# Kernel optimization log

Hardware: AMD Instinct MI355X
Metric: run time of the kernel (lower is better)

## Reference

```python
import jax, jax.numpy as jnp
import numpy as np

N = 30000      # nodes
E = 480000     # edges (before self loops)
DIN = 128      # dim_in
DH = 32        # dim_h (per-head out channels)
H1 = 8         # gat1 heads
H2 = 2         # gat2 heads
G = 64         # num graphs in batch
DOUT = 10      # dim_out
NEG_SLOPE = 0.2


def _glorot(key, shape):
    fan_in = shape[0]
    return jax.random.normal(key, shape, dtype=jnp.float32) / np.sqrt(fan_in)


def setup_inputs() -> dict:
    key = jax.random.key(0)
    ks = jax.random.split(key, 16)
    x = jax.random.normal(ks[0], (N, DIN), dtype=jnp.float32)
    edge_index = jax.random.randint(ks[1], (2, E), 0, N, dtype=jnp.int32)
    batch = jnp.sort(jax.random.randint(ks[2], (N,), 0, G, dtype=jnp.int32))
    # GATv2Conv layer 1: lin_l, lin_r (dim_in -> H1*DH), att (H1, DH), bias (H1*DH)
    W1l = _glorot(ks[3], (DIN, H1 * DH))
    W1r = _glorot(ks[4], (DIN, H1 * DH))
    a1 = _glorot(ks[5], (DH, H1)).T  # [H1, DH]
    b1 = jnp.zeros((H1 * DH,), dtype=jnp.float32)
    # GATv2Conv layer 2: (H1*DH -> H2*DH)
    W2l = _glorot(ks[6], (H1 * DH, H2 * DH))
    W2r = _glorot(ks[7], (H1 * DH, H2 * DH))
    a2 = _glorot(ks[8], (DH, H2)).T  # [H2, DH]
    b2 = jnp.zeros((H2 * DH,), dtype=jnp.float32)
    # MLP head: fc1(2*DH -> DH), fc2(DH -> DH//2), fc(DH//2 -> DOUT); stored [in,out]
    fc1_w = _glorot(ks[9], (2 * DH, DH)); fc1_b = jnp.zeros((DH,), jnp.float32)
    fc2_w = _glorot(ks[10], (DH, DH // 2)); fc2_b = jnp.zeros((DH // 2,), jnp.float32)
    fc_w = _glorot(ks[11], (DH // 2, DOUT)); fc_b = jnp.zeros((DOUT,), jnp.float32)
    return {"x": x, "edge_index": edge_index, "batch": batch,
            "W1l": W1l, "W1r": W1r, "a1": a1, "b1": b1,
            "W2l": W2l, "W2r": W2r, "a2": a2, "b2": b2,
            "fc1_w": fc1_w, "fc1_b": fc1_b, "fc2_w": fc2_w, "fc2_b": fc2_b,
            "fc_w": fc_w, "fc_b": fc_b}


def gatv2_conv(x, edge_index, Wl, Wr, att, bias, heads, dh, n):
    """PyG GATv2Conv: concat=True, add_self_loops=True, negative_slope=0.2."""
    src, dst = edge_index[0], edge_index[1]
    loop = jnp.arange(n, dtype=src.dtype)        # self loops (PyG default)
    src = jnp.concatenate([src, loop])
    dst = jnp.concatenate([dst, loop])
    xl = (x @ Wl).reshape(n, heads, dh)          # source transform
    xr = (x @ Wr).reshape(n, heads, dh)          # destination transform
    xj = xl[src]                                  # [Etot, H, dh] message features
    s = jax.nn.leaky_relu(xj + xr[dst], NEG_SLOPE)
    e = jnp.einsum('ehd,hd->eh', s, att)          # per-edge per-head score
    # segment softmax over incoming edges of each destination node
    m = jax.ops.segment_max(e, dst, num_segments=n)
    p = jnp.exp(e - m[dst])
    z = jax.ops.segment_sum(p, dst, num_segments=n)
    alpha = p / z[dst]                            # [Etot, H]
    out = jax.ops.segment_sum(xj * alpha[..., None], dst, num_segments=n)
    return out.reshape(n, heads * dh) + bias


def reference(x, edge_index, batch, W1l, W1r, a1, b1, W2l, W2r, a2, b2,
              fc1_w, fc1_b, fc2_w, fc2_b, fc_w, fc_b):
    h = gatv2_conv(x, edge_index, W1l, W1r, a1, b1, H1, DH, N)
    h = jax.nn.elu(h)
    h = gatv2_conv(h, edge_index, W2l, W2r, a2, b2, H2, DH, N)  # [N, 2*DH]
    # global_mean_pool
    sums = jax.ops.segment_sum(h, batch, num_segments=G)
    cnt = jax.ops.segment_sum(jnp.ones((N,), h.dtype), batch, num_segments=G)
    hg = sums / jnp.maximum(cnt, 1.0)[:, None]    # [G, 2*DH]
    x1 = jax.nn.relu(hg @ fc1_w + fc1_b)
    # dropout p=0.2 is identity in eval mode
    x2 = jax.nn.relu(x1 @ fc2_w + fc2_b)
    c = x2 @ fc_w + fc_b
    return (c, x2)
```

## Files before the change

kernel.cpp:

```cpp
#include <hip/hip_runtime.h>
#include <math.h>

#define DIN 128
#define DH  32
#define H1  8
#define H2  2
#define GNUM 64
#define DOUT 10
#define NEG_SLOPE 0.2f
#define SCAN_B 512

typedef __attribute__((ext_vector_type(8))) short sv8;
typedef __attribute__((ext_vector_type(4))) float fv4;

static __device__ __forceinline__ unsigned short f2bf(float f) {
    unsigned int u = __float_as_uint(f);
    unsigned int r = (u + 0x7fffu + ((u >> 16) & 1u)) >> 16;
    return (unsigned short)r;
}
static __device__ __forceinline__ float bf2f(unsigned short h) {
    return __uint_as_float(((unsigned int)h) << 16);
}


__global__ void k_prep(const float* __restrict__ x,
                       const float* __restrict__ W1l, const float* __restrict__ W1r,
                       const float* __restrict__ W2l, const float* __restrict__ W2r,
                       unsigned short* __restrict__ xgh, unsigned short* __restrict__ xgl,
                       short* __restrict__ B1th, short* __restrict__ B1tl,
                       short* __restrict__ B2th, short* __restrict__ B2tl,
                       int* __restrict__ zbase, int nz, int n) {
    int id = blockIdx.x * blockDim.x + threadIdx.x;
    if (id < nz) zbase[id] = 0;
    const int NX = n * 32;
    const int T1 = 512 * 128;
    const int T2 = 128 * 256;
    if (id < NX) {
        int m = id >> 5, j4 = id & 31;
        float4 v = *(const float4*)(x + (size_t)m * 128 + j4 * 4);
        unsigned short hx = f2bf(v.x), hy = f2bf(v.y), hz = f2bf(v.z), hw = f2bf(v.w);
        ushort4 hi; hi.x = hx; hi.y = hy; hi.z = hz; hi.w = hw;
        ushort4 lo;
        lo.x = f2bf(v.x - bf2f(hx)); lo.y = f2bf(v.y - bf2f(hy));
        lo.z = f2bf(v.z - bf2f(hz)); lo.w = f2bf(v.w - bf2f(hw));
        int R = m >> 4, r = m & 15;
        int C = j4 >> 3, q = (j4 >> 1) & 3, j = (j4 & 1) * 4;
        size_t o = ((size_t)(R * 4 + C) * 64 + q * 16 + r) * 8 + j;
        *(ushort4*)(xgh + o) = hi;
        *(ushort4*)(xgl + o) = lo;
    } else if (id < NX + T1) {
        int id1 = id - NX;
        int nn = id1 / 128, k = id1 - nn * 128;
        float v = (nn < 256) ? W1l[(size_t)k * 256 + nn] : W1r[(size_t)k * 256 + (nn - 256)];
        unsigned short h = f2bf(v);
        size_t o = (((size_t)(nn >> 4) * 4 + (k >> 5)) * 64 + ((k >> 3) & 3) * 16 + (nn & 15)) * 8 + (k & 7);
        B1th[o] = (short)h;
        B1tl[o] = (short)f2bf(v - bf2f(h));
    } else if (id < NX + T1 + T2) {
        int id2 = id - NX - T1;
        int nn = id2 / 256, k = id2 - nn * 256;
        float v = (nn < 64) ? W2l[(size_t)k * 64 + nn] : W2r[(size_t)k * 64 + (nn - 64)];
        unsigned short h = f2bf(v);
        size_t o = (((size_t)(nn >> 4) * 8 + (k >> 5)) * 64 + ((k >> 3) & 3) * 16 + (nn & 15)) * 8 + (k & 7);
        B2th[o] = (short)h;
        B2tl[o] = (short)f2bf(v - bf2f(h));
    }
}

__global__ void k_deg(const int* __restrict__ dst, int* __restrict__ deg, int E, int n) {
    int i = blockIdx.x * blockDim.x + threadIdx.x;
    if (i < E) {
        atomicAdd(&deg[dst[i]], 1);
    } else if (i < E + n) {
        atomicAdd(&deg[i - E], 1);
    }
}

__global__ __launch_bounds__(SCAN_B)
void k_scan_partial(const int* __restrict__ deg, int* __restrict__ bsum, int n) {
    int i = blockIdx.x * SCAN_B + threadIdx.x;
    int v = (i < n) ? deg[i] : 0;
    #pragma unroll
    for (int m = 32; m >= 1; m >>= 1) v += __shfl_xor(v, m);
    __shared__ int red[SCAN_B / 64];
    if ((threadIdx.x & 63) == 0) red[threadIdx.x >> 6] = v;
    __syncthreads();
    if (threadIdx.x == 0) {
        int s = 0;
        #pragma unroll
        for (int k = 0; k < SCAN_B / 64; ++k) s += red[k];
        bsum[blockIdx.x] = s;
    }
}

__global__ __launch_bounds__(SCAN_B)
void k_scan_apply(int* __restrict__ deg, int* __restrict__ cursor,
                  const int* __restrict__ bsum, int n, int nb) {
    __shared__ int buf[SCAN_B];
    __shared__ int pfx_s, tot_s;
    const int t = threadIdx.x, b = blockIdx.x;
    if (t < 64) {
        int v = (t < nb) ? bsum[t] : 0;
        int incl = v;
        #pragma unroll
        for (int o = 1; o < 64; o <<= 1) {
            int w = __shfl_up(incl, o);
            if (t >= o) incl += w;
        }
        int pfx = (b == 0) ? 0 : __shfl(incl, b - 1);
        int tot = __shfl(incl, nb - 1);
        if (t == 0) { pfx_s = pfx; tot_s = tot; }
    }
    int i = b * SCAN_B + t;
    int v = (i < n) ? deg[i] : 0;
    buf[t] = v;
    __syncthreads();
    for (int o = 1; o < SCAN_B; o <<= 1) {
        int a = (t >= o) ? buf[t - o] : 0;
        __syncthreads();
        buf[t] += a;
        __syncthreads();
    }
    int excl = buf[t] - v + pfx_s;
    if (i < n) { deg[i] = excl; cursor[i] = excl; }
    if (b == 0 && t == 0) deg[n] = tot_s;
}

__global__ void k_scatter(const int* __restrict__ src, const int* __restrict__ dst,
                          int* __restrict__ cursor, int* __restrict__ csr_src, int E, int n) {
    int i = blockIdx.x * blockDim.x + threadIdx.x;
    if (i < E) {
        int d = dst[i];
        int pos = atomicAdd(&cursor[d], 1);
        csr_src[pos] = src[i];
    } else if (i < E + n) {
        int v = i - E;
        int pos = atomicAdd(&cursor[v], 1);
        csr_src[pos] = v;
    }
}

__global__ __launch_bounds__(256, 2)
void k_gemm1(const unsigned short* __restrict__ Ah, const unsigned short* __restrict__ Al,
             const short* __restrict__ Bth, const short* __restrict__ Btl,
             unsigned short* __restrict__ C,
             int M, int Ntot) {
    __shared__ float smc[64 * 68];
    const int tid = threadIdx.x;
    const int lane = tid & 63;
    const int wid = tid >> 6;
    const int wm = wid & 1, wn = wid >> 1;
    const int m0 = blockIdx.x * 128;
    const int n0 = blockIdx.y * 128;
    const int l15 = lane & 15, q = lane >> 4;
    const int MR = (M >> 4) - 1;

    fv4 acc[4][4] = {};

    const unsigned short* ap[4];
    const unsigned short* alp[4];
    #pragma unroll
    for (int fm = 0; fm < 4; ++fm) {
        int R = (m0 >> 4) + wm * 4 + fm;
        if (R > MR) R = MR;
        ap[fm]  = Ah + ((size_t)R * 4 * 64 + lane) * 8;
        alp[fm] = Al + ((size_t)R * 4 * 64 + lane) * 8;
    }
    const short* bhp[4];
    const short* blp[4];
    #pragma unroll
    for (int fn = 0; fn < 4; ++fn) {
        int R = (n0 >> 4) + wn * 4 + fn;
        bhp[fn] = Bth + ((size_t)R * 4 * 64 + lane) * 8;
        blp[fn] = Btl + ((size_t)R * 4 * 64 + lane) * 8;
    }

    #pragma unroll
    for (int c = 0; c < 4; ++c) {
        const size_t co = (size_t)c * 512;
        sv8 ah[4], al[4], bh[4], bl[4];
        #pragma unroll
        for (int fn = 0; fn < 4; ++fn) {
            bh[fn] = *(const sv8*)(bhp[fn] + co);
            bl[fn] = *(const sv8*)(blp[fn] + co);
        }
        #pragma unroll
        for (int fm = 0; fm < 4; ++fm) {
            ah[fm] = *(const sv8*)(ap[fm] + co);
            al[fm] = *(const sv8*)(alp[fm] + co);
        }
        #pragma unroll
        for (int fm = 0; fm < 4; ++fm) {
            #pragma unroll
            for (int fn = 0; fn < 4; ++fn) {
                acc[fm][fn] = __builtin_amdgcn_mfma_f32_16x16x32_bf16(ah[fm], bh[fn], acc[fm][fn], 0, 0, 0);
                acc[fm][fn] = __builtin_amdgcn_mfma_f32_16x16x32_bf16(ah[fm], bl[fn], acc[fm][fn], 0, 0, 0);
                acc[fm][fn] = __builtin_amdgcn_mfma_f32_16x16x32_bf16(al[fm], bh[fn], acc[fm][fn], 0, 0, 0);
            }
        }
    }

    #pragma unroll
    for (int s = 0; s < 2; ++s) {
        #pragma unroll
        for (int cn = 0; cn < 2; ++cn) {
            __syncthreads();
            if (wm == s && wn == cn) {
                #pragma unroll
                for (int fm = 0; fm < 4; ++fm)
                    #pragma unroll
                    for (int fn = 0; fn < 4; ++fn)
                        #pragma unroll
                        for (int r = 0; r < 4; ++r)
                            smc[(fm * 16 + q * 4 + r) * 68 + fn * 16 + l15] = acc[fm][fn][r];
            }
            __syncthreads();
            int lr = tid >> 2;
            int grow = m0 + s * 64 + lr;
            if (grow < M) {
                #pragma unroll
                for (int k4 = 0; k4 < 4; ++k4) {
                    int jj = (tid & 3) + k4 * 4;
                    float4 vv = *(float4*)&smc[lr * 68 + jj * 4];
                    int gcol = n0 + cn * 64 + jj * 4;
                    ushort4 uu;
                    uu.x = f2bf(vv.x); uu.y = f2bf(vv.y);
                    uu.z = f2bf(vv.z); uu.w = f2bf(vv.w);
                    *(ushort4*)(C + (size_t)grow * Ntot + gcol) = uu;
                }
            }
        }
    }
}

__global__ __launch_bounds__(256, 2)
void k_gemm_bf(const unsigned short* __restrict__ A, const short* __restrict__ Bth,
               const short* __restrict__ Btl,
               unsigned short* __restrict__ C,
               int M, int Ntot) {
    __shared__ float smc[64 * 36];
    const int tid = threadIdx.x;
    const int lane = tid & 63;
    const int wid = tid >> 6;
    const int wm = wid & 1, wn = wid >> 1;
    const int m0 = blockIdx.x * 128;
    const int n0 = blockIdx.y * 64;
    const int l15 = lane & 15, q = lane >> 4;
    const int MR = (M >> 4) - 1;

    fv4 acc[4][2] = {};

    const unsigned short* ap[4];
    #pragma unroll
    for (int fm = 0; fm < 4; ++fm) {
        int R = (m0 >> 4) + wm * 4 + fm;
        if (R > MR) R = MR;
        ap[fm] = A + ((size_t)R * 8 * 64 + lane) * 8;
    }
    const short* bhp[2];
    const short* blp[2];
    #pragma unroll
    for (int fn = 0; fn < 2; ++fn) {
        int R = (n0 >> 4) + wn * 2 + fn;
        bhp[fn] = Bth + ((size_t)R * 8 * 64 + lane) * 8;
        blp[fn] = Btl + ((size_t)R * 8 * 64 + lane) * 8;
    }

    #pragma unroll 4
    for (int c = 0; c < 8; ++c) {
        const size_t co = (size_t)c * 512;
        sv8 ah[4], bh[2], bl[2];
        #pragma unroll
        for (int fn = 0; fn < 2; ++fn) {
            bh[fn] = *(const sv8*)(bhp[fn] + co);
            bl[fn] = *(const sv8*)(blp[fn] + co);
        }
        #pragma unroll
        for (int fm = 0; fm < 4; ++fm)
            ah[fm] = *(const sv8*)(ap[fm] + co);
        #pragma unroll
        for (int fm = 0; fm < 4; ++fm) {
            #pragma unroll
            for (int fn = 0; fn < 2; ++fn) {
                acc[fm][fn] = __builtin_amdgcn_mfma_f32_16x16x32_bf16(ah[fm], bh[fn], acc[fm][fn], 0, 0, 0);
                acc[fm][fn] = __builtin_amdgcn_mfma_f32_16x16x32_bf16(ah[fm], bl[fn], acc[fm][fn], 0, 0, 0);
            }
        }
    }

    #pragma unroll
    for (int s = 0; s < 2; ++s) {
        #pragma unroll
        for (int cn = 0; cn < 2; ++cn) {
            __syncthreads();
            if (wm == s && wn == cn) {
                #pragma unroll
                for (int fm = 0; fm < 4; ++fm)
                    #pragma unroll
                    for (int fn = 0; fn < 2; ++fn)
                        #pragma unroll
                        for (int r = 0; r < 4; ++r)
                            smc[(fm * 16 + q * 4 + r) * 36 + fn * 16 + l15] = acc[fm][fn][r];
            }
            __syncthreads();
            int lr = tid >> 2;
            int grow = m0 + s * 64 + lr;
            if (grow < M) {
                #pragma unroll
                for (int k4 = 0; k4 < 2; ++k4) {
                    int jj = (tid & 3) + k4 * 4;
                    float4 vv = *(float4*)&smc[lr * 36 + jj * 4];
                    int gcol = n0 + cn * 32 + jj * 4;
                    ushort4 uu;
                    uu.x = f2bf(vv.x); uu.y = f2bf(vv.y);
                    uu.z = f2bf(vv.z); uu.w = f2bf(vv.w);
                    *(ushort4*)(C + (size_t)grow * Ntot + gcol) = uu;
                }
            }
        }
    }
}

__global__ __launch_bounds__(256)
void k_edge1(const unsigned short* __restrict__ XLR,
             const int* __restrict__ offs, const int* __restrict__ csr,
             const float* __restrict__ att, const float* __restrict__ bias,
             unsigned short* __restrict__ out, int n) {
    const int tid = threadIdx.x;
    const int lane = tid & 63;
    const int v = blockIdx.x * 4 + (tid >> 6);
    if (v >= n) return;
    const int li = lane & 31;
    const int half = lane >> 5;
    const uint4* XL4 = (const uint4*)XLR;
    float av[8], xr[8];
    #pragma unroll
    for (int k = 0; k < 8; ++k) av[k] = att[li * 8 + k];
    {
        uint4 u = XL4[(size_t)v * 64 + 32 + li];
        xr[0] = __uint_as_float(u.x << 16);  xr[1] = __uint_as_float(u.x & 0xffff0000u);
        xr[2] = __uint_as_float(u.y << 16);  xr[3] = __uint_as_float(u.y & 0xffff0000u);
        xr[4] = __uint_as_float(u.z << 16);  xr[5] = __uint_as_float(u.z & 0xffff0000u);
        xr[6] = __uint_as_float(u.w << 16);  xr[7] = __uint_as_float(u.w & 0xffff0000u);
    }
    float z = 0.f;
    float acc[8] = {};
    const int e0 = offs[v], e1 = offs[v + 1];

    int j = e0 + half;
    bool val = (j < e1);
    int jj = val ? j : (e1 - 1);
    int src = csr[jj];
    uint4 u = XL4[(size_t)src * 64 + li];

    for (int base = e0; base < e1; base += 2) {
        int jn = j + 2;
        bool valn = (jn < e1);
        int jjn = valn ? jn : (e1 - 1);
        int srcn = csr[jjn];
        uint4 un = XL4[(size_t)srcn * 64 + li];

        float f[8];
        f[0] = __uint_as_float(u.x << 16);  f[1] = __uint_as_float(u.x & 0xffff0000u);
        f[2] = __uint_as_float(u.y << 16);  f[3] = __uint_as_float(u.y & 0xffff0000u);
        f[4] = __uint_as_float(u.z << 16);  f[5] = __uint_as_float(u.z & 0xffff0000u);
        f[6] = __uint_as_float(u.w << 16);  f[7] = __uint_as_float(u.w & 0xffff0000u);
        float s1 = 0.f, s2 = 0.f;
        #pragma unroll
        for (int k = 0; k < 8; ++k) {
            float t = f[k] + xr[k];
            s1 = fmaf(t, av[k], s1);
            s2 = fmaf(fabsf(t), av[k], s2);
        }
        float s = fmaf(0.6f, s1, 0.4f * s2);
        s += __shfl_xor(s, 1);
        s += __shfl_xor(s, 2);
        float w = val ? __expf(s) : 0.f;
        z += w;
        #pragma unroll
        for (int k = 0; k < 8; ++k) acc[k] = fmaf(w, f[k], acc[k]);

        u = un; val = valn; j = jn;
    }
    z += __shfl_xor(z, 32);
    #pragma unroll
    for (int k = 0; k < 8; ++k) acc[k] += __shfl_xor(acc[k], 32);
    if (half == 0) {
        const float rz = 1.f / z;
        unsigned int o[4];
        #pragma unroll
        for (int k2 = 0; k2 < 4; ++k2) {
            float lo = fmaf(acc[k2 * 2 + 0], rz, bias[li * 8 + k2 * 2 + 0]);
            float hi = fmaf(acc[k2 * 2 + 1], rz, bias[li * 8 + k2 * 2 + 1]);
            lo = (lo > 0.f) ? lo : (__expf(lo) - 1.f);
            hi = (hi > 0.f) ? hi : (__expf(hi) - 1.f);
            o[k2] = (unsigned int)f2bf(lo) | ((unsigned int)f2bf(hi) << 16);
        }
        uint4 ov = { o[0], o[1], o[2], o[3] };
        size_t po = (((size_t)(v >> 4) * 8 + (li >> 2)) * 64 + (li & 3) * 16 + (v & 15)) * 8;
        *(uint4*)(out + po) = ov;
    }
}

__global__ __launch_bounds__(256)
void k_edge2(const unsigned short* __restrict__ XLR,
             const int* __restrict__ offs, const int* __restrict__ csr,
             const float* __restrict__ att, const float* __restrict__ bias,
             float* __restrict__ out, int n) {
    const int tid = threadIdx.x;
    const int lane = tid & 63;
    const int v = blockIdx.x * 4 + (tid >> 6);
    if (v >= n) return;
    const int li = lane & 7;
    const int slot = lane >> 3;
    const uint4* XL4 = (const uint4*)XLR;
    float av[8], xr[8];
    #pragma unroll
    for (int k = 0; k < 8; ++k) av[k] = att[li * 8 + k];
    {
        uint4 u = XL4[(size_t)v * 16 + 8 + li];
        xr[0] = __uint_as_float(u.x << 16);  xr[1] = __uint_as_float(u.x & 0xffff0000u);
        xr[2] = __uint_as_float(u.y << 16);  xr[3] = __uint_as_float(u.y & 0xffff0000u);
        xr[4] = __uint_as_float(u.z << 16);  xr[5] = __uint_as_float(u.z & 0xffff0000u);
        xr[6] = __uint_as_float(u.w << 16);  xr[7] = __uint_as_float(u.w & 0xffff0000u);
    }
    float z = 0.f;
    float acc[8] = {};
    const int e0 = offs[v], e1 = offs[v + 1];

    int j = e0 + slot;
    bool val = (j < e1);
    int jj = val ? j : (e1 - 1);
    int src = csr[jj];
    uint4 u = XL4[(size_t)src * 16 + li];

    for (int base = e0; base < e1; base += 8) {
        int jn = j + 8;
        bool valn = (jn < e1);
        int jjn = valn ? jn : (e1 - 1);
        int srcn = csr[jjn];
        uint4 un = XL4[(size_t)srcn * 16 + li];

        float f[8];
        f[0] = __uint_as_float(u.x << 16);  f[1] = __uint_as_float(u.x & 0xffff0000u);
        f[2] = __uint_as_float(u.y << 16);  f[3] = __uint_as_float(u.y & 0xffff0000u);
        f[4] = __uint_as_float(u.z << 16);  f[5] = __uint_as_float(u.z & 0xffff0000u);
        f[6] = __uint_as_float(u.w << 16);  f[7] = __uint_as_float(u.w & 0xffff0000u);
        float s1 = 0.f, s2 = 0.f;
        #pragma unroll
        for (int k = 0; k < 8; ++k) {
            float t = f[k] + xr[k];
            s1 = fmaf(t, av[k], s1);
            s2 = fmaf(fabsf(t), av[k], s2);
        }
        float s = fmaf(0.6f, s1, 0.4f * s2);
        s += __shfl_xor(s, 1);
        s += __shfl_xor(s, 2);
        float w = val ? __expf(s) : 0.f;
        z += w;
        #pragma unroll
        for (int k = 0; k < 8; ++k) acc[k] = fmaf(w, f[k], acc[k]);

        u = un; val = valn; j = jn;
    }
    z += __shfl_xor(z, 8);  z += __shfl_xor(z, 16);  z += __shfl_xor(z, 32);
    #pragma unroll
    for (int k = 0; k < 8; ++k) {
        acc[k] += __shfl_xor(acc[k], 8);
        acc[k] += __shfl_xor(acc[k], 16);
        acc[k] += __shfl_xor(acc[k], 32);
    }
    if (slot == 0) {
        const float rz = 1.f / z;
        float o[8];
        #pragma unroll
        for (int k = 0; k < 8; ++k)
            o[k] = fmaf(acc[k], rz, bias[li * 8 + k]);
        float4 o0 = { o[0], o[1], o[2], o[3] };
        float4 o1 = { o[4], o[5], o[6], o[7] };
        *(float4*)(out + (size_t)v * 64 + li * 8 + 0) = o0;
        *(float4*)(out + (size_t)v * 64 + li * 8 + 4) = o1;
    }
}

__global__ __launch_bounds__(256)
void k_pool_mlp(const float* __restrict__ out2, const int* __restrict__ batch,
                const float* __restrict__ fc1w, const float* __restrict__ fc1b,
                const float* __restrict__ fc2w, const float* __restrict__ fc2b,
                const float* __restrict__ fcw,  const float* __restrict__ fcb,
                float* __restrict__ outc, float* __restrict__ outx2, int n) {
    const int g = blockIdx.x;
    const int t = threadIdx.x;
    const int lane = t & 63;
    const int w = t >> 6;
    __shared__ float red[4][64];
    __shared__ float hg_s[64];
    __shared__ float x1_s[32];
    __shared__ float x2_s[16];

    int lo = 0, hi = n;
    while (lo < hi) { int mid = (lo + hi) >> 1; if (batch[mid] < g) lo = mid + 1; else hi = mid; }
    const int start = lo;
    hi = n;
    while (lo < hi) { int mid = (lo + hi) >> 1; if (batch[mid] < g + 1) lo = mid + 1; else hi = mid; }
    const int end = lo;

    float s = 0.f;
    for (int v = start + w; v < end; v += 4)
        s += out2[(size_t)v * 64 + lane];
    red[w][lane] = s;
    __syncthreads();
    if (w == 0) {
        float tot = red[0][lane] + red[1][lane] + red[2][lane] + red[3][lane];
        float cnt = fmaxf((float)(end - start), 1.0f);
        hg_s[lane] = tot / cnt;
    }
    __syncthreads();
    if (t < 32) {
        float a = fc1b[t];
        #pragma unroll
        for (int k = 0; k < 64; ++k) a = fmaf(hg_s[k], fc1w[k * 32 + t], a);
        x1_s[t] = fmaxf(a, 0.f);
    }
    __syncthreads();
    if (t < 16) {
        float a = fc2b[t];
        #pragma unroll
        for (int k = 0; k < 32; ++k) a = fmaf(x1_s[k], fc2w[k * 16 + t], a);
        x2_s[t] = fmaxf(a, 0.f);
    }
    __syncthreads();
    if (t < DOUT) {
        float a = fcb[t];
        #pragma unroll
        for (int k = 0; k < 16; ++k) a = fmaf(x2_s[k], fcw[k * 10 + t], a);
        outc[g * DOUT + t] = a;
    }
    if (t < 16) outx2[g * 16 + t] = x2_s[t];
}

extern "C" void kernel_launch(void* const* d_in, const int* in_sizes, int n_in,
                              void* d_out, int out_size, void* d_ws, size_t ws_size,
                              hipStream_t stream) {
    const float* x    = (const float*)d_in[0];
    const int*   ei   = (const int*)d_in[1];
    const int*   batch= (const int*)d_in[2];
    const float* W1l  = (const float*)d_in[3];
    const float* W1r  = (const float*)d_in[4];
    const float* a1   = (const float*)d_in[5];
    const float* b1   = (const float*)d_in[6];
    const float* W2l  = (const float*)d_in[7];
    const float* W2r  = (const float*)d_in[8];
    const float* a2   = (const float*)d_in[9];
    const float* b2   = (const float*)d_in[10];
    const float* fc1w = (const float*)d_in[11];
    const float* fc1b = (const float*)d_in[12];
    const float* fc2w = (const float*)d_in[13];
    const float* fc2b = (const float*)d_in[14];
    const float* fcw  = (const float*)d_in[15];
    const float* fcb  = (const float*)d_in[16];

    const int N = in_sizes[2];
    const int E = in_sizes[1] / 2;
    const int ET = E + N;
    const int* esrc = ei;
    const int* edst = ei + E;
    const int NB = (N + SCAN_B - 1) / SCAN_B;

    char* ws = (char*)d_ws;
    size_t off = 0;
    unsigned short* xlr1b = (unsigned short*)(ws + off); off += (size_t)N * 512 * 2;
    unsigned short* h1b  = (unsigned short*)(ws + off);  off += (size_t)N * 256 * 2;
    float* out2 = (float*)(ws + off);            off += (size_t)N * 64 * 4;
    int*   deg   = (int*)(ws + off);             off += ((size_t)(N + 1) * 4 + 255) & ~255ull;
    int*   cursor= (int*)(ws + off);             off += ((size_t)N * 4 + 255) & ~255ull;
    int*   csr   = (int*)(ws + off);             off += ((size_t)ET * 4 + 255) & ~255ull;
    int*   bsum  = (int*)(ws + off);             off += ((size_t)(NB + 1) * 4 + 255) & ~255ull;
    short* B1th  = (short*)(ws + off);           off += (size_t)512 * 128 * 2;
    short* B1tl  = (short*)(ws + off);           off += (size_t)512 * 128 * 2;
    short* B2th  = (short*)(ws + off);           off += (size_t)128 * 256 * 2;
    short* B2tl  = (short*)(ws + off);           off += (size_t)128 * 256 * 2;
    unsigned short* xgh = (unsigned short*)(ws + off); off += (size_t)N * 128 * 2;
    unsigned short* xgl = (unsigned short*)(ws + off); off += (size_t)N * 128 * 2;
    unsigned short* xlr2b = xlr1b;
    (void)ws_size; (void)n_in; (void)out_size;

    float* outc  = (float*)d_out;
    float* outx2 = (float*)d_out + GNUM * DOUT;

    const int prep_tot = N * 32 + 512 * 128 + 128 * 256;
    k_prep<<<(prep_tot + 255) / 256, 256, 0, stream>>>(
        x, W1l, W1r, W2l, W2r, xgh, xgl, B1th, B1tl, B2th, B2tl, deg, N + 1, N);

    int tb = 256;
    int gb = (ET + tb - 1) / tb;
    k_deg<<<gb, tb, 0, stream>>>(edst, deg, E, N);
    k_scan_partial<<<NB, SCAN_B, 0, stream>>>(deg, bsum, N);
    k_scan_apply<<<NB, SCAN_B, 0, stream>>>(deg, cursor, bsum, N, NB);
    k_scatter<<<gb, tb, 0, stream>>>(esrc, edst, cursor, csr, E, N);

    dim3 g1((N + 127) / 128, 4);
    k_gemm1<<<g1, 256, 0, stream>>>(xgh, xgl, B1th, B1tl, xlr1b, N, 512);

    k_edge1<<<(N + 3) / 4, 256, 0, stream>>>(xlr1b, deg, csr, a1, b1, h1b, N);

    dim3 g2((N + 127) / 128, 2);
    k_gemm_bf<<<g2, 256, 0, stream>>>(h1b, B2th, B2tl, xlr2b, N, 128);

    k_edge2<<<(N + 3) / 4, 256, 0, stream>>>(xlr2b, deg, csr, a2, b2, out2, N);

    k_pool_mlp<<<GNUM, 256, 0, stream>>>(out2, batch, fc1w, fc1b, fc2w, fc2b,
                                         fcw, fcb, outc, outx2, N);
}
```

Measured before the change: 275.2 us.

## Split XL/XR buffers, deepen gather prefetch, and pack edge math into float2 ops

The combined XL|XR projection buffer is split into separate contiguous XL and XR arrays, so edge gathers read a compact 256- or 64-wide row instead of striding over 512- or 128-wide rows. The GEMM epilogues now stage a full 128-row tile in shared memory with fewer barriers and store 16-byte packed bf16 using v_cvt_pk_bf16_f32. The edge kernels prefetch two iterations ahead and use packed float2 FMA/max/min arithmetic for leaky-ReLU scoring. The log2e factor is folded into the attention weights so exp2 can replace exp. Shared memory per GEMM block doubles, which may affect occupancy.

```diff
diff --git a/kernel.cpp b/kernel.cpp
--- a/kernel.cpp
+++ b/kernel.cpp
@@ -12,6 +12,7 @@
 
 typedef __attribute__((ext_vector_type(8))) short sv8;
 typedef __attribute__((ext_vector_type(4))) float fv4;
+typedef __attribute__((ext_vector_type(2))) float f32x2;
 
 static __device__ __forceinline__ unsigned short f2bf(float f) {
     unsigned int u = __float_as_uint(f);
@@ -20,6 +21,17 @@
 }
 static __device__ __forceinline__ float bf2f(unsigned short h) {
     return __uint_as_float(((unsigned int)h) << 16);
+}
+static __device__ __forceinline__ unsigned int cvtpk(float lo, float hi) {
+    unsigned int r;
+    asm("v_cvt_pk_bf16_f32 %0, %1, %2" : "=v"(r) : "v"(lo), "v"(hi));
+    return r;
+}
+static __device__ __forceinline__ f32x2 up2(unsigned int w) {
+    f32x2 r;
+    r.x = __uint_as_float(w << 16);
+    r.y = __uint_as_float(w & 0xffff0000u);
+    return r;
 }
 
 
@@ -143,9 +155,9 @@
 __global__ __launch_bounds__(256, 2)
 void k_gemm1(const unsigned short* __restrict__ Ah, const unsigned short* __restrict__ Al,
              const short* __restrict__ Bth, const short* __restrict__ Btl,
-             unsigned short* __restrict__ C,
-             int M, int Ntot) {
-    __shared__ float smc[64 * 68];
+             unsigned short* __restrict__ XLo, unsigned short* __restrict__ XRo,
+             int M) {
+    __shared__ float smc[128 * 68];
     const int tid = threadIdx.x;
     const int lane = tid & 63;
     const int wid = tid >> 6;
@@ -201,33 +213,33 @@
     }
 
     #pragma unroll
-    for (int s = 0; s < 2; ++s) {
-        #pragma unroll
-        for (int cn = 0; cn < 2; ++cn) {
-            __syncthreads();
-            if (wm == s && wn == cn) {
+    for (int p = 0; p < 2; ++p) {
+        if (p) __syncthreads();
+        if (wn == p) {
+            #pragma unroll
+            for (int fm = 0; fm < 4; ++fm)
                 #pragma unroll
-                for (int fm = 0; fm < 4; ++fm)
+                for (int fn = 0; fn < 4; ++fn)
                     #pragma unroll
-                    for (int fn = 0; fn < 4; ++fn)
-                        #pragma unroll
-                        for (int r = 0; r < 4; ++r)
-                            smc[(fm * 16 + q * 4 + r) * 68 + fn * 16 + l15] = acc[fm][fn][r];
-            }
-            __syncthreads();
-            int lr = tid >> 2;
-            int grow = m0 + s * 64 + lr;
-            if (grow < M) {
-                #pragma unroll
-                for (int k4 = 0; k4 < 4; ++k4) {
-                    int jj = (tid & 3) + k4 * 4;
-                    float4 vv = *(float4*)&smc[lr * 68 + jj * 4];
-                    int gcol = n0 + cn * 64 + jj * 4;
-                    ushort4 uu;
-                    uu.x = f2bf(vv.x); uu.y = f2bf(vv.y);
-                    uu.z = f2bf(vv.z); uu.w = f2bf(vv.w);
-                    *(ushort4*)(C + (size_t)grow * Ntot + gcol) = uu;
-                }
+                    for (int r = 0; r < 4; ++r)
+                        smc[(wm * 64 + fm * 16 + q * 4 + r) * 68 + fn * 16 + l15] = acc[fm][fn][r];
+        }
+        __syncthreads();
+        int lr = tid >> 1;
+        int ch = (tid & 1) * 32;
+        int grow = m0 + lr;
+        if (grow < M) {
+            int colb = n0 + p * 64 + ch;
+            unsigned short* dst = (colb < 256)
+                ? XLo + (size_t)grow * 256 + colb
+                : XRo + (size_t)grow * 256 + (colb - 256);
+            #pragma unroll
+            for (int j = 0; j < 4; ++j) {
+                float4 a = *(float4*)&smc[lr * 68 + ch + j * 8];
+                float4 b = *(float4*)&smc[lr * 68 + ch + j * 8 + 4];
+                uint4 o = { cvtpk(a.x, a.y), cvtpk(a.z, a.w),
+                            cvtpk(b.x, b.y), cvtpk(b.z, b.w) };
+                *(uint4*)(dst + j * 8) = o;
             }
         }
     }
@@ -236,9 +248,9 @@
 __global__ __launch_bounds__(256, 2)
 void k_gemm_bf(const unsigned short* __restrict__ A, const short* __restrict__ Bth,
                const short* __restrict__ Btl,
-               unsigned short* __restrict__ C,
-               int M, int Ntot) {
-    __shared__ float smc[64 * 36];
+               unsigned short* __restrict__ XL2, unsigned short* __restrict__ XR2,
+               int M) {
+    __shared__ float smc[128 * 36];
     const int tid = threadIdx.x;
     const int lane = tid & 63;
     const int wid = tid >> 6;
@@ -289,40 +301,40 @@
     }
 
     #pragma unroll
-    for (int s = 0; s < 2; ++s) {
-        #pragma unroll
-        for (int cn = 0; cn < 2; ++cn) {
-            __syncthreads();
-            if (wm == s && wn == cn) {
+    for (int p = 0; p < 2; ++p) {
+        if (p) __syncthreads();
+        if (wn == p) {
+            #pragma unroll
+            for (int fm = 0; fm < 4; ++fm)
                 #pragma unroll
-                for (int fm = 0; fm < 4; ++fm)
+                for (int fn = 0; fn < 2; ++fn)
                     #pragma unroll
-                    for (int fn = 0; fn < 2; ++fn)
-                        #pragma unroll
-                        for (int r = 0; r < 4; ++r)
-                            smc[(fm * 16 + q * 4 + r) * 36 + fn * 16 + l15] = acc[fm][fn][r];
+                    for (int r = 0; r < 4; ++r)
+                        smc[(wm * 64 + fm * 16 + q * 4 + r) * 36 + fn * 16 + l15] = acc[fm][fn][r];
+        }
+        __syncthreads();
+        int lr = tid >> 1;
+        int ch = (tid & 1) * 16;
+        int grow = m0 + lr;
+        if (grow < M) {
+            int colb = n0 + p * 32 + ch;
+            unsigned short* dst = (colb < 64)
+                ? XL2 + (size_t)grow * 64 + colb
+                : XR2 + (size_t)grow * 64 + (colb - 64);
+            #pragma unroll
+            for (int j = 0; j < 2; ++j) {
+                float4 a = *(float4*)&smc[lr * 36 + ch + j * 8];
+                float4 b = *(float4*)&smc[lr * 36 + ch + j * 8 + 4];
+                uint4 o = { cvtpk(a.x, a.y), cvtpk(a.z, a.w),
+                            cvtpk(b.x, b.y), cvtpk(b.z, b.w) };
+                *(uint4*)(dst + j * 8) = o;
             }
-            __syncthreads();
-            int lr = tid >> 2;
-            int grow = m0 + s * 64 + lr;
-            if (grow < M) {
-                #pragma unroll
-                for (int k4 = 0; k4 < 2; ++k4) {
-                    int jj = (tid & 3) + k4 * 4;
-                    float4 vv = *(float4*)&smc[lr * 36 + jj * 4];
-                    int gcol = n0 + cn * 32 + jj * 4;
-                    ushort4 uu;
-                    uu.x = f2bf(vv.x); uu.y = f2bf(vv.y);
-                    uu.z = f2bf(vv.z); uu.w = f2bf(vv.w);
-                    *(ushort4*)(C + (size_t)grow * Ntot + gcol) = uu;
-                }
-            }
         }
     }
 }
 
 __global__ __launch_bounds__(256)
-void k_edge1(const unsigned short* __restrict__ XLR,
+void k_edge1(const unsigned short* __restrict__ XL, const unsigned short* __restrict__ XR,
              const int* __restrict__ offs, const int* __restrict__ csr,
              const float* __restrict__ att, const float* __restrict__ bias,
              unsigned short* __restrict__ out, int n) {
@@ -332,69 +344,83 @@
     if (v >= n) return;
     const int li = lane & 31;
     const int half = lane >> 5;
-    const uint4* XL4 = (const uint4*)XLR;
-    float av[8], xr[8];
-    #pragma unroll
-    for (int k = 0; k < 8; ++k) av[k] = att[li * 8 + k];
+    const uint4* XL4 = (const uint4*)XL;
+    const uint4* XR4 = (const uint4*)XR;
+    const float LOG2E = 1.4426950408889634f;
+    f32x2 av[4], xr[4];
+    #pragma unroll
+    for (int k = 0; k < 4; ++k) {
+        av[k].x = att[li * 8 + 2 * k] * LOG2E;
+        av[k].y = att[li * 8 + 2 * k + 1] * LOG2E;
+    }
     {
-        uint4 u = XL4[(size_t)v * 64 + 32 + li];
-        xr[0] = __uint_as_float(u.x << 16);  xr[1] = __uint_as_float(u.x & 0xffff0000u);
-        xr[2] = __uint_as_float(u.y << 16);  xr[3] = __uint_as_float(u.y & 0xffff0000u);
-        xr[4] = __uint_as_float(u.z << 16);  xr[5] = __uint_as_float(u.z & 0xffff0000u);
-        xr[6] = __uint_as_float(u.w << 16);  xr[7] = __uint_as_float(u.w & 0xffff0000u);
+        uint4 u = XR4[(size_t)v * 32 + li];
+        xr[0] = up2(u.x); xr[1] = up2(u.y); xr[2] = up2(u.z); xr[3] = up2(u.w);
     }
     float z = 0.f;
-    float acc[8] = {};
+    f32x2 acc[4] = {};
     const int e0 = offs[v], e1 = offs[v + 1];
-
-    int j = e0 + half;
-    bool val = (j < e1);
-    int jj = val ? j : (e1 - 1);
-    int src = csr[jj];
-    uint4 u = XL4[(size_t)src * 64 + li];
-
+    const int el = e1 - 1;
+
+    int j0 = e0 + half;
+    int c0 = csr[j0 < e1 ? j0 : el];
+    uint4 u0 = XL4[(size_t)c0 * 32 + li];
+    int j1 = j0 + 2;
+    int c1 = csr[j1 < e1 ? j1 : el];
+    uint4 u1 = XL4[(size_t)c1 * 32 + li];
+    int j2 = j0 + 4;
+    int c2 = csr[j2 < e1 ? j2 : el];
+
+    #pragma unroll 2
     for (int base = e0; base < e1; base += 2) {
-        int jn = j + 2;
-        bool valn = (jn < e1);
-        int jjn = valn ? jn : (e1 - 1);
-        int srcn = csr[jjn];
-        uint4 un = XL4[(size_t)srcn * 64 + li];
-
-        float f[8];
-        f[0] = __uint_as_float(u.x << 16);  f[1] = __uint_as_float(u.x & 0xffff0000u);
-        f[2] = __uint_as_float(u.y << 16);  f[3] = __uint_as_float(u.y & 0xffff0000u);
-        f[4] = __uint_as_float(u.z << 16);  f[5] = __uint_as_float(u.z & 0xffff0000u);
-        f[6] = __uint_as_float(u.w << 16);  f[7] = __uint_as_float(u.w & 0xffff0000u);
-        float s1 = 0.f, s2 = 0.f;
-        #pragma unroll
-        for (int k = 0; k < 8; ++k) {
-            float t = f[k] + xr[k];
-            s1 = fmaf(t, av[k], s1);
-            s2 = fmaf(fabsf(t), av[k], s2);
-        }
-        float s = fmaf(0.6f, s1, 0.4f * s2);
+        uint4 u2 = XL4[(size_t)c2 * 32 + li];
+        int j3 = j2 + 2;
+        int c3 = csr[j3 < e1 ? j3 : el];
+
+        f32x2 f0 = up2(u0.x), f1 = up2(u0.y), f2 = up2(u0.z), f3 = up2(u0.w);
+        const f32x2 zz = { 0.f, 0.f };
+        f32x2 sp = zz, sm = zz, t;
+        t = f0 + xr[0];
+        sp = __builtin_elementwise_fma(__builtin_elementwise_max(t, zz), av[0], sp);
+        sm = __builtin_elementwise_fma(__builtin_elementwise_min(t, zz), av[0], sm);
+        t = f1 + xr[1];
+        sp = __builtin_elementwise_fma(__builtin_elementwise_max(t, zz), av[1], sp);
+        sm = __builtin_elementwise_fma(__builtin_elementwise_min(t, zz), av[1], sm);
+        t = f2 + xr[2];
+        sp = __builtin_elementwise_fma(__builtin_elementwise_max(t, zz), av[2], sp);
+        sm = __builtin_elementwise_fma(__builtin_elementwise_min(t, zz), av[2], sm);
+        t = f3 + xr[3];
+        sp = __builtin_elementwise_fma(__builtin_elementwise_max(t, zz), av[3], sp);
+        sm = __builtin_elementwise_fma(__builtin_elementwise_min(t, zz), av[3], sm);
+        float s = (sp.x + sp.y) + 0.2f * (sm.x + sm.y);
         s += __shfl_xor(s, 1);
         s += __shfl_xor(s, 2);
-        float w = val ? __expf(s) : 0.f;
+        float w = (j0 < e1) ? exp2f(s) : 0.f;
         z += w;
-        #pragma unroll
-        for (int k = 0; k < 8; ++k) acc[k] = fmaf(w, f[k], acc[k]);
-
-        u = un; val = valn; j = jn;
+        f32x2 ww = { w, w };
+        acc[0] = __builtin_elementwise_fma(f0, ww, acc[0]);
+        acc[1] = __builtin_elementwise_fma(f1, ww, acc[1]);
+        acc[2] = __builtin_elementwise_fma(f2, ww, acc[2]);
+        acc[3] = __builtin_elementwise_fma(f3, ww, acc[3]);
+
+        u0 = u1; u1 = u2;
+        j0 = j1; j1 = j2; j2 = j3; c2 = c3;
     }
     z += __shfl_xor(z, 32);
-    #pragma unroll
-    for (int k = 0; k < 8; ++k) acc[k] += __shfl_xor(acc[k], 32);
+    float a8[8] = { acc[0].x, acc[0].y, acc[1].x, acc[1].y,
+                    acc[2].x, acc[2].y, acc[3].x, acc[3].y };
+    #pragma unroll
+    for (int k = 0; k < 8; ++k) a8[k] += __shfl_xor(a8[k], 32);
     if (half == 0) {
         const float rz = 1.f / z;
         unsigned int o[4];
         #pragma unroll
         for (int k2 = 0; k2 < 4; ++k2) {
-            float lo = fmaf(acc[k2 * 2 + 0], rz, bias[li * 8 + k2 * 2 + 0]);
-            float hi = fmaf(acc[k2 * 2 + 1], rz, bias[li * 8 + k2 * 2 + 1]);
+            float lo = fmaf(a8[2 * k2 + 0], rz, bias[li * 8 + 2 * k2 + 0]);
+            float hi = fmaf(a8[2 * k2 + 1], rz, bias[li * 8 + 2 * k2 + 1]);
             lo = (lo > 0.f) ? lo : (__expf(lo) - 1.f);
             hi = (hi > 0.f) ? hi : (__expf(hi) - 1.f);
-            o[k2] = (unsigned int)f2bf(lo) | ((unsigned int)f2bf(hi) << 16);
+            o[k2] = cvtpk(lo, hi);
         }
         uint4 ov = { o[0], o[1], o[2], o[3] };
         size_t po = (((size_t)(v >> 4) * 8 + (li >> 2)) * 64 + (li & 3) * 16 + (v & 15)) * 8;
@@ -403,7 +429,7 @@
 }
 
 __global__ __launch_bounds__(256)
-void k_edge2(const unsigned short* __restrict__ XLR,
+void k_edge2(const unsigned short* __restrict__ XL, const unsigned short* __restrict__ XR,
              const int* __restrict__ offs, const int* __restrict__ csr,
              const float* __restrict__ att, const float* __restrict__ bias,
              float* __restrict__ out, int n) {
@@ -413,69 +439,83 @@
     if (v >= n) return;
     const int li = lane & 7;
     const int slot = lane >> 3;
-    const uint4* XL4 = (const uint4*)XLR;
-    float av[8], xr[8];
-    #pragma unroll
-    for (int k = 0; k < 8; ++k) av[k] = att[li * 8 + k];
+    const uint4* XL4 = (const uint4*)XL;
+    const uint4* XR4 = (const uint4*)XR;
+    const float LOG2E = 1.4426950408889634f;
+    f32x2 av[4], xr[4];
+    #pragma unroll
+    for (int k = 0; k < 4; ++k) {
+        av[k].x = att[li * 8 + 2 * k] * LOG2E;
+        av[k].y = att[li * 8 + 2 * k + 1] * LOG2E;
+    }
     {
-        uint4 u = XL4[(size_t)v * 16 + 8 + li];
-        xr[0] = __uint_as_float(u.x << 16);  xr[1] = __uint_as_float(u.x & 0xffff0000u);
-        xr[2] = __uint_as_float(u.y << 16);  xr[3] = __uint_as_float(u.y & 0xffff0000u);
-        xr[4] = __uint_as_float(u.z << 16);  xr[5] = __uint_as_float(u.z & 0xffff0000u);
-        xr[6] = __uint_as_float(u.w << 16);  xr[7] = __uint_as_float(u.w & 0xffff0000u);
+        uint4 u = XR4[(size_t)v * 8 + li];
+        xr[0] = up2(u.x); xr[1] = up2(u.y); xr[2] = up2(u.z); xr[3] = up2(u.w);
     }
     float z = 0.f;
-    float acc[8] = {};
+    f32x2 acc[4] = {};
     const int e0 = offs[v], e1 = offs[v + 1];
-
-    int j = e0 + slot;
-    bool val = (j < e1);
-    int jj = val ? j : (e1 - 1);
-    int src = csr[jj];
-    uint4 u = XL4[(size_t)src * 16 + li];
-
+    const int el = e1 - 1;
+
+    int j0 = e0 + slot;
+    int c0 = csr[j0 < e1 ? j0 : el];
+    uint4 u0 = XL4[(size_t)c0 * 8 + li];
+    int j1 = j0 + 8;
+    int c1 = csr[j1 < e1 ? j1 : el];
+    uint4 u1 = XL4[(size_t)c1 * 8 + li];
+    int j2 = j0 + 16;
+    int c2 = csr[j2 < e1 ? j2 : el];
+
+    #pragma unroll 2
     for (int base = e0; base < e1; base += 8) {
-        int jn = j + 8;
-        bool valn = (jn < e1);
-        int jjn = valn ? jn : (e1 - 1);
-        int srcn = csr[jjn];
-        uint4 un = XL4[(size_t)srcn * 16 + li];
-
-        float f[8];
-        f[0] = __uint_as_float(u.x << 16);  f[1] = __uint_as_float(u.x & 0xffff0000u);
-        f[2] = __uint_as_float(u.y << 16);  f[3] = __uint_as_float(u.y & 0xffff0000u);
-        f[4] = __uint_as_float(u.z << 16);  f[5] = __uint_as_float(u.z & 0xffff0000u);
-        f[6] = __uint_as_float(u.w << 16);  f[7] = __uint_as_float(u.w & 0xffff0000u);
-        float s1 = 0.f, s2 = 0.f;
-        #pragma unroll
-        for (int k = 0; k < 8; ++k) {
-            float t = f[k] + xr[k];
-            s1 = fmaf(t, av[k], s1);
-            s2 = fmaf(fabsf(t), av[k], s2);
-        }
-        float s = fmaf(0.6f, s1, 0.4f * s2);
+        uint4 u2 = XL4[(size_t)c2 * 8 + li];
+        int j3 = j2 + 8;
+        int c3 = csr[j3 < e1 ? j3 : el];
+
+        f32x2 f0 = up2(u0.x), f1 = up2(u0.y), f2 = up2(u0.z), f3 = up2(u0.w);
+        const f32x2 zz = { 0.f, 0.f };
+        f32x2 sp = zz, sm = zz, t;
+        t = f0 + xr[0];
+        sp = __builtin_elementwise_fma(__builtin_elementwise_max(t, zz), av[0], sp);
+        sm = __builtin_elementwise_fma(__builtin_elementwise_min(t, zz), av[0], sm);
+        t = f1 + xr[1];
+        sp = __builtin_elementwise_fma(__builtin_elementwise_max(t, zz), av[1], sp);
+        sm = __builtin_elementwise_fma(__builtin_elementwise_min(t, zz), av[1], sm);
+        t = f2 + xr[2];
+        sp = __builtin_elementwise_fma(__builtin_elementwise_max(t, zz), av[2], sp);
+        sm = __builtin_elementwise_fma(__builtin_elementwise_min(t, zz), av[2], sm);
+        t = f3 + xr[3];
+        sp = __builtin_elementwise_fma(__builtin_elementwise_max(t, zz), av[3], sp);
+        sm = __builtin_elementwise_fma(__builtin_elementwise_min(t, zz), av[3], sm);
+        float s = (sp.x + sp.y) + 0.2f * (sm.x + sm.y);
         s += __shfl_xor(s, 1);
         s += __shfl_xor(s, 2);
-        float w = val ? __expf(s) : 0.f;
+        float w = (j0 < e1) ? exp2f(s) : 0.f;
         z += w;
-        #pragma unroll
-        for (int k = 0; k < 8; ++k) acc[k] = fmaf(w, f[k], acc[k]);
-
-        u = un; val = valn; j = jn;
+        f32x2 ww = { w, w };
+        acc[0] = __builtin_elementwise_fma(f0, ww, acc[0]);
+        acc[1] = __builtin_elementwise_fma(f1, ww, acc[1]);
+        acc[2] = __builtin_elementwise_fma(f2, ww, acc[2]);
+        acc[3] = __builtin_elementwise_fma(f3, ww, acc[3]);
+
+        u0 = u1; u1 = u2;
+        j0 = j1; j1 = j2; j2 = j3; c2 = c3;
     }
     z += __shfl_xor(z, 8);  z += __shfl_xor(z, 16);  z += __shfl_xor(z, 32);
+    float a8[8] = { acc[0].x, acc[0].y, acc[1].x, acc[1].y,
+                    acc[2].x, acc[2].y, acc[3].x, acc[3].y };
     #pragma unroll
     for (int k = 0; k < 8; ++k) {
-        acc[k] += __shfl_xor(acc[k], 8);
-        acc[k] += __shfl_xor(acc[k], 16);
-        acc[k] += __shfl_xor(acc[k], 32);
+        a8[k] += __shfl_xor(a8[k], 8);
+        a8[k] += __shfl_xor(a8[k], 16);
+        a8[k] += __shfl_xor(a8[k], 32);
     }
     if (slot == 0) {
         const float rz = 1.f / z;
         float o[8];
         #pragma unroll
         for (int k = 0; k < 8; ++k)
-            o[k] = fmaf(acc[k], rz, bias[li * 8 + k]);
+            o[k] = fmaf(a8[k], rz, bias[li * 8 + k]);
         float4 o0 = { o[0], o[1], o[2], o[3] };
         float4 o1 = { o[4], o[5], o[6], o[7] };
         *(float4*)(out + (size_t)v * 64 + li * 8 + 0) = o0;
@@ -569,8 +609,9 @@
 
     char* ws = (char*)d_ws;
     size_t off = 0;
-    unsigned short* xlr1b = (unsigned short*)(ws + off); off += (size_t)N * 512 * 2;
-    unsigned short* h1b  = (unsigned short*)(ws + off);  off += (size_t)N * 256 * 2;
+    unsigned short* XL1 = (unsigned short*)(ws + off); off += (size_t)N * 256 * 2;
+    unsigned short* XR1 = (unsigned short*)(ws + off); off += (size_t)N * 256 * 2;
+    unsigned short* h1b = (unsigned short*)(ws + off); off += (size_t)N * 256 * 2;
     float* out2 = (float*)(ws + off);            off += (size_t)N * 64 * 4;
     int*   deg   = (int*)(ws + off);             off += ((size_t)(N + 1) * 4 + 255) & ~255ull;
     int*   cursor= (int*)(ws + off);             off += ((size_t)N * 4 + 255) & ~255ull;
@@ -582,7 +623,8 @@
     short* B2tl  = (short*)(ws + off);           off += (size_t)128 * 256 * 2;
     unsigned short* xgh = (unsigned short*)(ws + off); off += (size_t)N * 128 * 2;
     unsigned short* xgl = (unsigned short*)(ws + off); off += (size_t)N * 128 * 2;
-    unsigned short* xlr2b = xlr1b;
+    unsigned short* XL2 = XL1;
+    unsigned short* XR2 = XL1 + (size_t)N * 64;
     (void)ws_size; (void)n_in; (void)out_size;
 
     float* outc  = (float*)d_out;
@@ -600,14 +642,14 @@
     k_scatter<<<gb, tb, 0, stream>>>(esrc, edst, cursor, csr, E, N);
 
     dim3 g1((N + 127) / 128, 4);
-    k_gemm1<<<g1, 256, 0, stream>>>(xgh, xgl, B1th, B1tl, xlr1b, N, 512);
-
-    k_edge1<<<(N + 3) / 4, 256, 0, stream>>>(xlr1b, deg, csr, a1, b1, h1b, N);
+    k_gemm1<<<g1, 256, 0, stream>>>(xgh, xgl, B1th, B1tl, XL1, XR1, N);
+
+    k_edge1<<<(N + 3) / 4, 256, 0, stream>>>(XL1, XR1, deg, csr, a1, b1, h1b, N);
 
     dim3 g2((N + 127) / 128, 2);
-    k_gemm_bf<<<g2, 256, 0, stream>>>(h1b, B2th, B2tl, xlr2b, N, 128);
-
-    k_edge2<<<(N + 3) / 4, 256, 0, stream>>>(xlr2b, deg, csr, a2, b2, out2, N);
+    k_gemm_bf<<<g2, 256, 0, stream>>>(h1b, B2th, B2tl, XL2, XR2, N);
+
+    k_edge2<<<(N + 3) / 4, 256, 0, stream>>>(XL2, XR2, deg, csr, a2, b2, out2, N);
 
     k_pool_mlp<<<GNUM, 256, 0, stream>>>(out2, batch, fc1w, fc1b, fc2w, fc2b,
                                          fcw, fcb, outc, outx2, N);
```

Result: slower. 295.5 us (+7.4%).
